# Optimization experiments

Hardware: AMD Instinct MI355X
Metric: run time of the kernel (lower is better)

Reference implementation:

```python
import jax, jax.numpy as jnp
import numpy as np


def conv1x1(x, w, b):
    # x: [B, Cin, D, H, W], w: [Cout, Cin], b: [Cout]
    return jnp.einsum('bcdhw,oc->bodhw', x, w) + b[None, :, None, None, None]


def setup_inputs() -> dict:
    key = jax.random.key(0)
    ks = jax.random.split(key, 9)
    B, C, D, H, W = 2, 64, 16, 16, 16
    Cc = 64          # context_dim
    C8 = C // 8      # inner attention dim
    s = 0.05
    return {
        'x': jax.random.normal(ks[0], (B, C, D, H, W), jnp.float32),
        'context': jax.random.normal(ks[1], (B, Cc, D, H, W), jnp.float32),
        'Wq': jax.random.normal(ks[2], (C8, C), jnp.float32) * s,
        'bq': jax.random.normal(ks[3], (C8,), jnp.float32) * s,
        'Wk': jax.random.normal(ks[4], (C8, Cc), jnp.float32) * s,
        'bk': jax.random.normal(ks[5], (C8,), jnp.float32) * s,
        'Wv': jax.random.normal(ks[6], (C, Cc), jnp.float32) * s,
        'bv': jax.random.normal(ks[7], (C,), jnp.float32) * s,
        'gamma': jax.random.normal(ks[8], (1,), jnp.float32) * s,
    }


def reference(x, context, Wq, bq, Wk, bk, Wv, bv, gamma):
    B, C, D, H, W = x.shape
    N = D * H * W
    q = conv1x1(x, Wq, bq).reshape(B, -1, N)        # [B, C/8, N]
    k = conv1x1(context, Wk, bk).reshape(B, -1, N)  # [B, C/8, N]
    v = conv1x1(context, Wv, bv).reshape(B, C, N)   # [B, C, N]
    # energy[b, n, m] = q[:, :, n] . k[:, :, m]  (no scaling, as in source)
    energy = jnp.einsum('bcn,bcm->bnm', q, k)       # [B, N, N]
    attn = jax.nn.softmax(energy, axis=-1)
    # out = v @ attn^T : out[b, c, n] = sum_m v[b, c, m] * attn[b, n, m]
    out = jnp.einsum('bcm,bnm->bcn', v, attn).reshape(B, C, D, H, W)
    return gamma[0] * out + x
```

## Files before the change

kernel.cpp:

```cpp
#include <hip/hip_runtime.h>

#define NTOK 4096

typedef __attribute__((ext_vector_type(8))) short short8;
typedef __attribute__((ext_vector_type(4))) float f32x4;
typedef __attribute__((ext_vector_type(4))) unsigned int uint4v;

__device__ __forceinline__ unsigned short f2bf(float f) {
    unsigned u = __float_as_uint(f);
    u += 0x7fffu + ((u >> 16) & 1u);
    return (unsigned short)(u >> 16);
}

__device__ __forceinline__ float bf2f(unsigned short h) {
    return __uint_as_float((unsigned)h << 16);
}

__device__ __forceinline__ unsigned int pk2(float lo, float hi) {
    return __builtin_amdgcn_perm(__float_as_uint(hi), __float_as_uint(lo), 0x07060302u);
}

__global__ __launch_bounds__(256) void proj(
    const float* __restrict__ x, const float* __restrict__ ctx,
    const float* __restrict__ Wq, const float* __restrict__ bq,
    const float* __restrict__ Wk, const float* __restrict__ bk,
    const float* __restrict__ Wv, const float* __restrict__ bv,
    unsigned short* __restrict__ qbf, unsigned short* __restrict__ kbf,
    unsigned short* __restrict__ vtp)
{
    __shared__ float sW[16 * 64];
    __shared__ float sB[16];
    int tid  = threadIdx.x;
    int ogrp = blockIdx.z;
    int b    = blockIdx.y;
    int n0   = blockIdx.x * 64;

    if (ogrp == 0) {
        for (int i = tid; i < 1024; i += 256)
            sW[i] = (i < 512) ? Wq[i] : Wk[i - 512];
        if (tid < 16) sB[tid] = (tid < 8) ? bq[tid] : bk[tid - 8];
    } else {
        for (int i = tid; i < 1024; i += 256)
            sW[i] = Wv[(ogrp - 1) * 1024 + i];
        if (tid < 16) sB[tid] = bv[(ogrp - 1) * 16 + tid];
    }
    __syncthreads();

    int nn   = tid & 63;
    int osub = tid >> 6;
    const float* inp = (ogrp == 0 && osub < 2) ? x : ctx;
    const float* ip  = inp + (size_t)b * 64 * NTOK + n0 + nn;

    float a0 = sB[osub * 4 + 0], a1 = sB[osub * 4 + 1];
    float a2 = sB[osub * 4 + 2], a3 = sB[osub * 4 + 3];
#pragma unroll 16
    for (int c = 0; c < 64; ++c) {
        float val = ip[(size_t)c * NTOK];
        a0 += sW[(osub * 4 + 0) * 64 + c] * val;
        a1 += sW[(osub * 4 + 1) * 64 + c] * val;
        a2 += sW[(osub * 4 + 2) * 64 + c] * val;
        a3 += sW[(osub * 4 + 3) * 64 + c] * val;
    }
    float av[4] = {a0, a1, a2, a3};

    if (ogrp == 0) {
        bool isq = osub < 2;
        float sc = isq ? 1.4426950408889634f : 1.0f;
        unsigned short* dst = isq ? qbf : kbf;
        int half = osub & 1;
        ushort4 pk = {f2bf(av[0] * sc), f2bf(av[1] * sc), f2bf(av[2] * sc), f2bf(av[3] * sc)};
        *(ushort4*)&dst[((size_t)b * NTOK + n0 + nn) * 8 + half * 4] = pk;
    } else {
        int cbase = (ogrp - 1) * 16 + osub * 4;
        int m  = n0 + nn;
        int g  = m & ~31;
        int mm = m & 31;
        int p  = ((mm >> 2) & 3) * 8 + (mm >> 4) * 4 + (mm & 3);
#pragma unroll
        for (int j = 0; j < 4; ++j)
            vtp[((size_t)b * 64 + cbase + j) * NTOK + g + p] = f2bf(av[j]);
    }
}

__global__ __launch_bounds__(256, 2) void attn7(
    const unsigned short* __restrict__ qbf, const unsigned short* __restrict__ kbf,
    const unsigned short* __restrict__ vtp,
    unsigned short* __restrict__ partO, float* __restrict__ partL)
{
    __shared__ float sOc[4][16][68];
    __shared__ float sL[4][64];

    int tid  = threadIdx.x;
    int w    = tid >> 6, lane = tid & 63;
    int n    = lane & 15, quad = lane >> 4;
    int nt   = blockIdx.x;
    int b    = blockIdx.y;
    int qz   = blockIdx.z;
    int n0   = nt * 64;

    const f32x4 z4 = {0.f, 0.f, 0.f, 0.f};
    const short8 z8 = {0, 0, 0, 0, 0, 0, 0, 0};

    short8 bq[4];
#pragma unroll
    for (int g = 0; g < 4; ++g)
        bq[g] = (quad == 0)
            ? *(const short8*)&qbf[((size_t)b * NTOK + n0 + g * 16 + n) * 8]
            : z8;

    const unsigned short* kb = kbf + (size_t)b * NTOK * 8;
    const unsigned short* vb = vtp + (size_t)b * 64 * NTOK;
    int mwbase = qz * 512 + w * 128;

    f32x4 acc[4][4];
#pragma unroll
    for (int g = 0; g < 4; ++g)
#pragma unroll
        for (int ct = 0; ct < 4; ++ct) acc[g][ct] = z4;
    float lsum[4] = {0.f, 0.f, 0.f, 0.f};

    for (int h = 0; h < 2; ++h) {
        int m0 = mwbase + h * 64;

        short8 kf0 = (quad == 0) ? *(const short8*)&kb[(size_t)(m0 + 0 * 16 + n) * 8] : z8;
        short8 kf1 = (quad == 0) ? *(const short8*)&kb[(size_t)(m0 + 1 * 16 + n) * 8] : z8;
        short8 kf2 = (quad == 0) ? *(const short8*)&kb[(size_t)(m0 + 2 * 16 + n) * 8] : z8;
        short8 kf3 = (quad == 0) ? *(const short8*)&kb[(size_t)(m0 + 3 * 16 + n) * 8] : z8;

        short8 af[2][4];
#pragma unroll
        for (int s = 0; s < 2; ++s)
#pragma unroll
            for (int ct = 0; ct < 4; ++ct)
                af[s][ct] = *(const short8*)&vb[(size_t)(ct * 16 + n) * NTOK
                                                + m0 + s * 32 + quad * 8];

#pragma unroll
        for (int g = 0; g < 4; ++g) {
            f32x4 sa0 = __builtin_amdgcn_mfma_f32_16x16x32_bf16(kf0, bq[g], z4, 0, 0, 0);
            f32x4 sa1 = __builtin_amdgcn_mfma_f32_16x16x32_bf16(kf1, bq[g], z4, 0, 0, 0);
            f32x4 sa2 = __builtin_amdgcn_mfma_f32_16x16x32_bf16(kf2, bq[g], z4, 0, 0, 0);
            f32x4 sa3 = __builtin_amdgcn_mfma_f32_16x16x32_bf16(kf3, bq[g], z4, 0, 0, 0);

            float e00 = __builtin_amdgcn_exp2f(sa0[0]), e01 = __builtin_amdgcn_exp2f(sa0[1]);
            float e02 = __builtin_amdgcn_exp2f(sa0[2]), e03 = __builtin_amdgcn_exp2f(sa0[3]);
            float e10 = __builtin_amdgcn_exp2f(sa1[0]), e11 = __builtin_amdgcn_exp2f(sa1[1]);
            float e12 = __builtin_amdgcn_exp2f(sa1[2]), e13 = __builtin_amdgcn_exp2f(sa1[3]);
            float e20 = __builtin_amdgcn_exp2f(sa2[0]), e21 = __builtin_amdgcn_exp2f(sa2[1]);
            float e22 = __builtin_amdgcn_exp2f(sa2[2]), e23 = __builtin_amdgcn_exp2f(sa2[3]);
            float e30 = __builtin_amdgcn_exp2f(sa3[0]), e31 = __builtin_amdgcn_exp2f(sa3[1]);
            float e32 = __builtin_amdgcn_exp2f(sa3[2]), e33 = __builtin_amdgcn_exp2f(sa3[3]);
            lsum[g] += ((e00 + e01) + (e02 + e03)) + ((e10 + e11) + (e12 + e13))
                     + ((e20 + e21) + (e22 + e23)) + ((e30 + e31) + (e32 + e33));

            uint4v t0, t1;
            t0[0] = pk2(e00, e01); t0[1] = pk2(e02, e03);
            t0[2] = pk2(e10, e11); t0[3] = pk2(e12, e13);
            t1[0] = pk2(e20, e21); t1[1] = pk2(e22, e23);
            t1[2] = pk2(e30, e31); t1[3] = pk2(e32, e33);
            short8 pf0 = __builtin_bit_cast(short8, t0);
            short8 pf1 = __builtin_bit_cast(short8, t1);

            acc[g][0] = __builtin_amdgcn_mfma_f32_16x16x32_bf16(af[0][0], pf0, acc[g][0], 0, 0, 0);
            acc[g][1] = __builtin_amdgcn_mfma_f32_16x16x32_bf16(af[0][1], pf0, acc[g][1], 0, 0, 0);
            acc[g][2] = __builtin_amdgcn_mfma_f32_16x16x32_bf16(af[0][2], pf0, acc[g][2], 0, 0, 0);
            acc[g][3] = __builtin_amdgcn_mfma_f32_16x16x32_bf16(af[0][3], pf0, acc[g][3], 0, 0, 0);
            acc[g][0] = __builtin_amdgcn_mfma_f32_16x16x32_bf16(af[1][0], pf1, acc[g][0], 0, 0, 0);
            acc[g][1] = __builtin_amdgcn_mfma_f32_16x16x32_bf16(af[1][1], pf1, acc[g][1], 0, 0, 0);
            acc[g][2] = __builtin_amdgcn_mfma_f32_16x16x32_bf16(af[1][2], pf1, acc[g][2], 0, 0, 0);
            acc[g][3] = __builtin_amdgcn_mfma_f32_16x16x32_bf16(af[1][3], pf1, acc[g][3], 0, 0, 0);
        }
    }

#pragma unroll
    for (int g = 0; g < 4; ++g) {
        float l = lsum[g];
        l += __shfl_xor(l, 16);
        l += __shfl_xor(l, 32);
        if (lane < 16) sL[w][g * 16 + n] = l;
    }

    unsigned short* pO = partO + ((size_t)((b * 64 + nt) * 8 + qz)) * 4096;
    float*          pL = partL + ((size_t)((b * 64 + nt) * 8 + qz)) * 64;

#pragma unroll
    for (int ct = 0; ct < 4; ++ct) {
        if (ct) __syncthreads();
#pragma unroll
        for (int g = 0; g < 4; ++g)
#pragma unroll
            for (int r = 0; r < 4; ++r)
                sOc[w][quad * 4 + r][g * 16 + n] = acc[g][ct][r];
        __syncthreads();
        for (int i = tid; i < 1024; i += 256) {
            int c16 = i >> 6, nn2 = i & 63;
            float s = sOc[0][c16][nn2] + sOc[1][c16][nn2]
                    + sOc[2][c16][nn2] + sOc[3][c16][nn2];
            pO[ct * 1024 + i] = f2bf(s);
        }
    }
    if (tid < 64)
        pL[tid] = sL[0][tid] + sL[1][tid] + sL[2][tid] + sL[3][tid];
}

__global__ __launch_bounds__(256) void mergeq(
    const unsigned short* __restrict__ partO, const float* __restrict__ partL,
    const float* __restrict__ x, const float* __restrict__ gamma,
    float* __restrict__ out)
{
    int tid = threadIdx.x;
    int nt  = blockIdx.x;
    int b   = blockIdx.y;
    int c   = tid >> 2;
    int j   = tid & 3;

    const unsigned short* pOb = partO + ((size_t)((b * 64 + nt) * 8)) * 4096;
    const float*          pLb = partL + ((size_t)((b * 64 + nt) * 8)) * 64;
    float g = gamma[0];
#pragma unroll
    for (int nq = 0; nq < 4; ++nq) {
        int ns = j * 16 + nq * 4;
        float4 o = {0.f, 0.f, 0.f, 0.f};
        float4 L = {0.f, 0.f, 0.f, 0.f};
#pragma unroll
        for (int qz = 0; qz < 8; ++qz) {
            ushort4 ov = *(const ushort4*)&pOb[qz * 4096 + c * 64 + ns];
            float4  lv = *(const float4*)&pLb[qz * 64 + ns];
            o.x += bf2f(ov.x); o.y += bf2f(ov.y);
            o.z += bf2f(ov.z); o.w += bf2f(ov.w);
            L.x += lv.x; L.y += lv.y; L.z += lv.z; L.w += lv.w;
        }
        size_t ob = ((size_t)b * 64 + c) * NTOK + nt * 64 + ns;
        float4 xv = *(const float4*)&x[ob];
        float4 res;
        res.x = g * (o.x / L.x) + xv.x;
        res.y = g * (o.y / L.y) + xv.y;
        res.z = g * (o.z / L.z) + xv.z;
        res.w = g * (o.w / L.w) + xv.w;
        *(float4*)&out[ob] = res;
    }
}

extern "C" void kernel_launch(void* const* d_in, const int* in_sizes, int n_in,
                              void* d_out, int out_size, void* d_ws, size_t ws_size,
                              hipStream_t stream) {
    const float* x     = (const float*)d_in[0];
    const float* ctx   = (const float*)d_in[1];
    const float* Wq    = (const float*)d_in[2];
    const float* bq    = (const float*)d_in[3];
    const float* Wk    = (const float*)d_in[4];
    const float* bk    = (const float*)d_in[5];
    const float* Wv    = (const float*)d_in[6];
    const float* bv    = (const float*)d_in[7];
    const float* gamma = (const float*)d_in[8];
    float* out = (float*)d_out;

    unsigned short* qbf   = (unsigned short*)d_ws;
    unsigned short* kbf   = qbf + 2 * NTOK * 8;
    unsigned short* vtp   = kbf + 2 * NTOK * 8;
    unsigned short* partO = vtp + 2 * 64 * NTOK;
    float*          partL = (float*)(partO + (size_t)2 * 64 * 8 * 4096);

    proj<<<dim3(64, 2, 5), 256, 0, stream>>>(x, ctx, Wq, bq, Wk, bk, Wv, bv, qbf, kbf, vtp);
    attn7<<<dim3(NTOK / 64, 2, 8), 256, 0, stream>>>(qbf, kbf, vtp, partO, partL);
    mergeq<<<dim3(NTOK / 64, 2), 256, 0, stream>>>(partO, partL, x, gamma, out);
}
```

Baseline: 100.7 us.

## Fuse merge into attention via atomic last-block reduction and restructure projection

Removes the separate merge kernel: each attention block increments a per-tile atomic counter, and the last of the eight split blocks does the cross-split reduction, normalisation and residual add. The projection kernel is reorganised into two z-slices with 512 threads, so each context load feeds both K and all V channels at once. V is now written in a fragment-ready tiled layout so the attention kernel reads it with one contiguous short8 per lane. This saves a kernel launch and redundant context reads. In exchange it adds atomics and fences, tail work serialised on the last block, and a counter reset placed inside the projection kernel.

```diff
diff --git a/kernel.cpp b/kernel.cpp
--- a/kernel.cpp
+++ b/kernel.cpp
@@ -20,75 +20,88 @@
     return __builtin_amdgcn_perm(__float_as_uint(hi), __float_as_uint(lo), 0x07060302u);
 }
 
-__global__ __launch_bounds__(256) void proj(
+__global__ __launch_bounds__(512) void proj2(
     const float* __restrict__ x, const float* __restrict__ ctx,
     const float* __restrict__ Wq, const float* __restrict__ bq,
     const float* __restrict__ Wk, const float* __restrict__ bk,
     const float* __restrict__ Wv, const float* __restrict__ bv,
     unsigned short* __restrict__ qbf, unsigned short* __restrict__ kbf,
-    unsigned short* __restrict__ vtp)
+    unsigned short* __restrict__ vtp, int* __restrict__ cnt)
 {
-    __shared__ float sW[16 * 64];
-    __shared__ float sB[16];
-    int tid  = threadIdx.x;
-    int ogrp = blockIdx.z;
-    int b    = blockIdx.y;
-    int n0   = blockIdx.x * 64;
-
-    if (ogrp == 0) {
-        for (int i = tid; i < 1024; i += 256)
-            sW[i] = (i < 512) ? Wq[i] : Wk[i - 512];
-        if (tid < 16) sB[tid] = (tid < 8) ? bq[tid] : bk[tid - 8];
-    } else {
-        for (int i = tid; i < 1024; i += 256)
-            sW[i] = Wv[(ogrp - 1) * 1024 + i];
-        if (tid < 16) sB[tid] = bv[(ogrp - 1) * 16 + tid];
-    }
+    __shared__ float sWv[64 * 64];
+    __shared__ float sWk[8 * 64];
+    __shared__ float sbv[64], sbk[8];
+
+    int tid = threadIdx.x;
+    int nt  = blockIdx.x;
+    int b   = blockIdx.y;
+    int z   = blockIdx.z;
+    int n0  = nt * 64;
+    int nn  = tid & 63;
+    int osub = tid >> 6;
+
+    if (z == 1) {
+        if (nt == 0 && b == 0 && tid < 128) cnt[tid] = 0;
+        if (tid < 512) { if (tid < 512) sWk[0] = sWk[0]; }
+        for (int i = tid; i < 512; i += 512) sWk[i] = Wq[i];
+        if (tid < 8) sbk[tid] = bq[tid];
+        __syncthreads();
+        const float* xp = x + (size_t)b * 64 * NTOK + n0 + nn;
+        float a = sbk[osub];
+#pragma unroll 16
+        for (int c = 0; c < 64; ++c)
+            a += sWk[osub * 64 + c] * xp[(size_t)c * NTOK];
+        qbf[((size_t)b * NTOK + n0 + nn) * 8 + osub] = f2bf(a * 1.4426950408889634f);
+        return;
+    }
+
+    for (int i = tid; i < 4096; i += 512) sWv[i] = Wv[i];
+    if (tid < 512) sWk[tid] = Wk[tid];
+    if (tid < 64) sbv[tid] = bv[tid];
+    else if (tid >= 64 && tid < 72) sbk[tid - 64] = bk[tid - 64];
     __syncthreads();
 
-    int nn   = tid & 63;
-    int osub = tid >> 6;
-    const float* inp = (ogrp == 0 && osub < 2) ? x : ctx;
-    const float* ip  = inp + (size_t)b * 64 * NTOK + n0 + nn;
-
-    float a0 = sB[osub * 4 + 0], a1 = sB[osub * 4 + 1];
-    float a2 = sB[osub * 4 + 2], a3 = sB[osub * 4 + 3];
-#pragma unroll 16
+    const float* cp = ctx + (size_t)b * 64 * NTOK + n0 + nn;
+    float av[8];
+#pragma unroll
+    for (int j = 0; j < 8; ++j) av[j] = sbv[osub * 8 + j];
+    float ak = sbk[osub];
+#pragma unroll 8
     for (int c = 0; c < 64; ++c) {
-        float val = ip[(size_t)c * NTOK];
-        a0 += sW[(osub * 4 + 0) * 64 + c] * val;
-        a1 += sW[(osub * 4 + 1) * 64 + c] * val;
-        a2 += sW[(osub * 4 + 2) * 64 + c] * val;
-        a3 += sW[(osub * 4 + 3) * 64 + c] * val;
-    }
-    float av[4] = {a0, a1, a2, a3};
-
-    if (ogrp == 0) {
-        bool isq = osub < 2;
-        float sc = isq ? 1.4426950408889634f : 1.0f;
-        unsigned short* dst = isq ? qbf : kbf;
-        int half = osub & 1;
-        ushort4 pk = {f2bf(av[0] * sc), f2bf(av[1] * sc), f2bf(av[2] * sc), f2bf(av[3] * sc)};
-        *(ushort4*)&dst[((size_t)b * NTOK + n0 + nn) * 8 + half * 4] = pk;
-    } else {
-        int cbase = (ogrp - 1) * 16 + osub * 4;
-        int m  = n0 + nn;
-        int g  = m & ~31;
-        int mm = m & 31;
-        int p  = ((mm >> 2) & 3) * 8 + (mm >> 4) * 4 + (mm & 3);
-#pragma unroll
-        for (int j = 0; j < 4; ++j)
-            vtp[((size_t)b * 64 + cbase + j) * NTOK + g + p] = f2bf(av[j]);
-    }
-}
-
-__global__ __launch_bounds__(256, 2) void attn7(
+        float v = cp[(size_t)c * NTOK];
+        ak += sWk[osub * 64 + c] * v;
+#pragma unroll
+        for (int j = 0; j < 8; ++j)
+            av[j] += sWv[(osub * 8 + j) * 64 + c] * v;
+    }
+
+    kbf[((size_t)b * NTOK + n0 + nn) * 8 + osub] = f2bf(ak);
+
+    int m  = n0 + nn;
+    int T  = m >> 5;
+    int mm = m & 31;
+    int p  = ((mm >> 2) & 3) * 8 + (mm >> 4) * 4 + (mm & 3);
+    int qd = p >> 3, j2 = p & 7;
+    unsigned short* vB = vtp + (size_t)b * 64 * NTOK;
+#pragma unroll
+    for (int j = 0; j < 8; ++j) {
+        int c    = osub * 8 + j;
+        int ctv  = c >> 4;
+        int lanev = (c & 15) + 16 * qd;
+        vB[(((size_t)T * 4 + ctv) * 64 + lanev) * 8 + j2] = f2bf(av[j]);
+    }
+}
+
+__global__ __launch_bounds__(256, 2) void attn9(
     const unsigned short* __restrict__ qbf, const unsigned short* __restrict__ kbf,
     const unsigned short* __restrict__ vtp,
-    unsigned short* __restrict__ partO, float* __restrict__ partL)
+    unsigned short* __restrict__ partO, float* __restrict__ partL,
+    int* __restrict__ cnt, const float* __restrict__ x,
+    const float* __restrict__ gamma, float* __restrict__ out)
 {
     __shared__ float sOc[4][16][68];
     __shared__ float sL[4][64];
+    __shared__ int sOld;
 
     int tid  = threadIdx.x;
     int w    = tid >> 6, lane = tid & 63;
@@ -121,6 +134,7 @@
 
     for (int h = 0; h < 2; ++h) {
         int m0 = mwbase + h * 64;
+        int Tb = m0 >> 5;
 
         short8 kf0 = (quad == 0) ? *(const short8*)&kb[(size_t)(m0 + 0 * 16 + n) * 8] : z8;
         short8 kf1 = (quad == 0) ? *(const short8*)&kb[(size_t)(m0 + 1 * 16 + n) * 8] : z8;
@@ -132,8 +146,7 @@
         for (int s = 0; s < 2; ++s)
 #pragma unroll
             for (int ct = 0; ct < 4; ++ct)
-                af[s][ct] = *(const short8*)&vb[(size_t)(ct * 16 + n) * NTOK
-                                                + m0 + s * 32 + quad * 8];
+                af[s][ct] = *(const short8*)&vb[(((size_t)(Tb + s) * 4 + ct) * 64 + lane) * 8];
 
 #pragma unroll
         for (int g = 0; g < 4; ++g) {
@@ -201,31 +214,28 @@
     }
     if (tid < 64)
         pL[tid] = sL[0][tid] + sL[1][tid] + sL[2][tid] + sL[3][tid];
-}
-
-__global__ __launch_bounds__(256) void mergeq(
-    const unsigned short* __restrict__ partO, const float* __restrict__ partL,
-    const float* __restrict__ x, const float* __restrict__ gamma,
-    float* __restrict__ out)
-{
-    int tid = threadIdx.x;
-    int nt  = blockIdx.x;
-    int b   = blockIdx.y;
-    int c   = tid >> 2;
-    int j   = tid & 3;
+
+    __threadfence();
+    if (tid == 0)
+        sOld = __hip_atomic_fetch_add(&cnt[b * 64 + nt], 1,
+                                      __ATOMIC_ACQ_REL, __HIP_MEMORY_SCOPE_AGENT);
+    __syncthreads();
+    if (sOld != 7) return;
 
     const unsigned short* pOb = partO + ((size_t)((b * 64 + nt) * 8)) * 4096;
     const float*          pLb = partL + ((size_t)((b * 64 + nt) * 8)) * 64;
-    float g = gamma[0];
+    float gm = gamma[0];
+    int c = tid >> 2;
+    int j = tid & 3;
 #pragma unroll
     for (int nq = 0; nq < 4; ++nq) {
         int ns = j * 16 + nq * 4;
         float4 o = {0.f, 0.f, 0.f, 0.f};
         float4 L = {0.f, 0.f, 0.f, 0.f};
 #pragma unroll
-        for (int qz = 0; qz < 8; ++qz) {
-            ushort4 ov = *(const ushort4*)&pOb[qz * 4096 + c * 64 + ns];
-            float4  lv = *(const float4*)&pLb[qz * 64 + ns];
+        for (int q8 = 0; q8 < 8; ++q8) {
+            ushort4 ov = *(const ushort4*)&pOb[q8 * 4096 + c * 64 + ns];
+            float4  lv = *(const float4*)&pLb[q8 * 64 + ns];
             o.x += bf2f(ov.x); o.y += bf2f(ov.y);
             o.z += bf2f(ov.z); o.w += bf2f(ov.w);
             L.x += lv.x; L.y += lv.y; L.z += lv.z; L.w += lv.w;
@@ -233,10 +243,10 @@
         size_t ob = ((size_t)b * 64 + c) * NTOK + nt * 64 + ns;
         float4 xv = *(const float4*)&x[ob];
         float4 res;
-        res.x = g * (o.x / L.x) + xv.x;
-        res.y = g * (o.y / L.y) + xv.y;
-        res.z = g * (o.z / L.z) + xv.z;
-        res.w = g * (o.w / L.w) + xv.w;
+        res.x = gm * (o.x / L.x) + xv.x;
+        res.y = gm * (o.y / L.y) + xv.y;
+        res.z = gm * (o.z / L.z) + xv.z;
+        res.w = gm * (o.w / L.w) + xv.w;
         *(float4*)&out[ob] = res;
     }
 }
@@ -260,8 +270,10 @@
     unsigned short* vtp   = kbf + 2 * NTOK * 8;
     unsigned short* partO = vtp + 2 * 64 * NTOK;
     float*          partL = (float*)(partO + (size_t)2 * 64 * 8 * 4096);
-
-    proj<<<dim3(64, 2, 5), 256, 0, stream>>>(x, ctx, Wq, bq, Wk, bk, Wv, bv, qbf, kbf, vtp);
-    attn7<<<dim3(NTOK / 64, 2, 8), 256, 0, stream>>>(qbf, kbf, vtp, partO, partL);
-    mergeq<<<dim3(NTOK / 64, 2), 256, 0, stream>>>(partO, partL, x, gamma, out);
-}
+    int*            cnt   = (int*)(partL + 2 * 64 * 8 * 64);
+
+    proj2<<<dim3(64, 2, 2), 512, 0, stream>>>(x, ctx, Wq, bq, Wk, bk, Wv, bv,
+                                              qbf, kbf, vtp, cnt);
+    attn9<<<dim3(NTOK / 64, 2, 8), 256, 0, stream>>>(qbf, kbf, vtp, partO, partL,
+                                                     cnt, x, gamma, out);
+}
```

Measured after the change: 188.6 us. +87.3%, slower.
